# Performance work log

Hardware: AMD Instinct MI355X
Metric: run time of the kernel (lower is better)

Reference implementation:

```python
import jax, jax.numpy as jnp
import numpy as np

# Model / context constants (prefill path with 2 equal-length sequences)
B, S = 2, 2048            # batch, seq_len (cu_seqlens_q = cu_seqlens_k = [0, S, 2S])
H, KV, HD = 32, 8, 128    # num_heads, num_kv_heads, head_dim
SCALE = HD ** -0.5
NUM_SLOTS = 8192          # KV-cache token slots
DKV = KV * HD
N = B * S


def setup_inputs() -> dict:
    key = jax.random.key(0)
    k1, k2, k3 = jax.random.split(key, 3)
    return {
        "q": jax.random.normal(k1, (N, H * HD), jnp.float32),
        "k": jax.random.normal(k2, (N, DKV), jnp.float32),
        "v": jax.random.normal(k3, (N, DKV), jnp.float32),
        "k_cache": jnp.zeros((NUM_SLOTS, DKV), jnp.float32),
        "v_cache": jnp.zeros((NUM_SLOTS, DKV), jnp.float32),
        "slot_mapping": jnp.arange(N, dtype=jnp.int32),
    }


def reference(q, k, v, k_cache, v_cache, slot_mapping):
    # --- store_kvcache: fused scatter-store of new K/V into the paged cache ---
    k_cache = k_cache.at[slot_mapping].set(k)   # [num_slots, KV*hd]
    v_cache = v_cache.at[slot_mapping].set(v)

    # --- paged prefill: keys/values read back from cache via slot table ---
    kk = k_cache[slot_mapping].reshape(B, S, KV, HD)
    vv = v_cache[slot_mapping].reshape(B, S, KV, HD)
    qh = q.reshape(B, S, H, HD)

    # GQA: each KV head serves H // KV query heads
    G = H // KV
    kk = jnp.repeat(kk, G, axis=2)  # [B, S, H, hd]
    vv = jnp.repeat(vv, G, axis=2)

    scores = jnp.einsum('bqhd,bkhd->bhqk', qh, kk) * SCALE  # [B, H, S, S]
    causal = jnp.tril(jnp.ones((S, S), dtype=bool))
    neg = jnp.asarray(jnp.finfo(scores.dtype).min, scores.dtype)
    scores = jnp.where(causal[None, None], scores, neg)
    p = jax.nn.softmax(scores, axis=-1)
    o = jnp.einsum('bhqk,bkhd->bqhd', p, vv)  # [B, S, H, hd]
    return o.reshape(N, H * HD)
```

## Files before the change

### kernel.cpp

```cpp
#include <hip/hip_runtime.h>

typedef _Float16 half8 __attribute__((ext_vector_type(8)));
typedef _Float16 half2v __attribute__((ext_vector_type(2)));
typedef float f32x4 __attribute__((ext_vector_type(4)));

#define SEQ_LEN 2048
#define N_GQ 4
#define HD 128
#define DQ 4096
#define DKV 1024
#define ATT_SCALE 0.08838834764831845f

__global__ __launch_bounds__(512, 2) void attn_fwd(
    const float* __restrict__ qg, const float* __restrict__ kg,
    const float* __restrict__ vg, float* __restrict__ og)
{
    __shared__ char smem[65536];
    char* const Kb = smem;
    char* const Vb = smem + 16384;
    const int tid  = threadIdx.x;
    const int w    = tid >> 6;
    const int lane = tid & 63;
    const int lg   = lane >> 4;
    const int lr   = lane & 15;
    char* const Pb = smem + 32768 + w * 4096;

    const int kvh  = blockIdx.y;
    const int seq0 = (int)blockIdx.z * SEQ_LEN;
    const int head = kvh * N_GQ + (w >> 1);

    for (int rep = 0; rep < 2; ++rep) {
        const int qt = rep ? (31 - (int)blockIdx.x) : (int)blockIdx.x;
        const int q0 = qt * 64;
        const int qw = q0 + (w & 1) * 32;

        half8 qf[2][4];
        #pragma unroll
        for (int mq = 0; mq < 2; ++mq) {
            const int row = qw + mq * 16 + lr;
            const float* qp = qg + (size_t)(seq0 + row) * DQ + head * HD + lg * 8;
            #pragma unroll
            for (int kc = 0; kc < 4; ++kc) {
                f32x4 a = *(const f32x4*)(qp + kc * 32);
                f32x4 b = *(const f32x4*)(qp + kc * 32 + 4);
                half8 h;
                #pragma unroll
                for (int i = 0; i < 4; ++i) {
                    h[i]     = (_Float16)(a[i] * ATT_SCALE);
                    h[i + 4] = (_Float16)(b[i] * ATT_SCALE);
                }
                qf[mq][kc] = h;
            }
        }

        f32x4 oa[2][8];
        #pragma unroll
        for (int mq = 0; mq < 2; ++mq)
            #pragma unroll
            for (int dt = 0; dt < 8; ++dt)
                oa[mq][dt] = (f32x4){0.f, 0.f, 0.f, 0.f};
        float mrow[2][4], lrow[2][4];
        #pragma unroll
        for (int mq = 0; mq < 2; ++mq)
            #pragma unroll
            for (int r = 0; r < 4; ++r) { mrow[mq][r] = -1e30f; lrow[mq][r] = 0.f; }

        const int ntiles = qt + 1;
        for (int kvt = 0; kvt < ntiles; ++kvt) {
            const int kv0 = kvt * 64;
            __syncthreads();

            {
                const int r = tid >> 3, p = tid & 7;
                const float* kp = kg + (size_t)(seq0 + kv0 + r) * DKV + kvh * HD + p * 16;
                f32x4 f0 = *(const f32x4*)(kp);
                f32x4 f1 = *(const f32x4*)(kp + 4);
                f32x4 f2 = *(const f32x4*)(kp + 8);
                f32x4 f3 = *(const f32x4*)(kp + 12);
                half8 h0, h1;
                #pragma unroll
                for (int i = 0; i < 4; ++i) {
                    h0[i] = (_Float16)f0[i]; h0[i + 4] = (_Float16)f1[i];
                    h1[i] = (_Float16)f2[i]; h1[i + 4] = (_Float16)f3[i];
                }
                const int s0 = (p * 2)     ^ (r & 7);
                const int s1 = (p * 2 + 1) ^ (r & 7);
                *(half8*)(Kb + r * 256 + s0 * 16) = h0;
                *(half8*)(Kb + r * 256 + s1 * 16) = h1;
            }
            {
                const int r2 = (tid & 31) * 2, p = tid >> 5;
                const float* vp = vg + (size_t)(seq0 + kv0 + r2) * DKV + kvh * HD + p * 8;
                f32x4 a0 = *(const f32x4*)(vp);
                f32x4 a1 = *(const f32x4*)(vp + 4);
                f32x4 b0 = *(const f32x4*)(vp + DKV);
                f32x4 b1 = *(const f32x4*)(vp + DKV + 4);
                #pragma unroll
                for (int c = 0; c < 8; ++c) {
                    const int d = p * 8 + c;
                    half2v hv;
                    hv[0] = (_Float16)(c < 4 ? a0[c] : a1[c - 4]);
                    hv[1] = (_Float16)(c < 4 ? b0[c] : b1[c - 4]);
                    const int byt = (r2 * 2) ^ ((d & 7) << 4);
                    *(half2v*)(Vb + d * 128 + byt) = hv;
                }
            }
            __syncthreads();

            f32x4 sc[2][4];
            #pragma unroll
            for (int mq = 0; mq < 2; ++mq)
                #pragma unroll
                for (int nk = 0; nk < 4; ++nk)
                    sc[mq][nk] = (f32x4){0.f, 0.f, 0.f, 0.f};
            #pragma unroll
            for (int nk = 0; nk < 4; ++nk) {
                const int krow = nk * 16 + lr;
                half8 kf[4];
                #pragma unroll
                for (int kc = 0; kc < 4; ++kc) {
                    const int byt = (kc * 64 + lg * 16) ^ ((krow & 7) << 4);
                    kf[kc] = *(const half8*)(Kb + krow * 256 + byt);
                }
                #pragma unroll
                for (int mq = 0; mq < 2; ++mq)
                    #pragma unroll
                    for (int kc = 0; kc < 4; ++kc)
                        sc[mq][nk] = __builtin_amdgcn_mfma_f32_16x16x32_f16(
                            qf[mq][kc], kf[kc], sc[mq][nk], 0, 0, 0);
            }

            if (kvt == ntiles - 1) {
                #pragma unroll
                for (int mq = 0; mq < 2; ++mq)
                    #pragma unroll
                    for (int nk = 0; nk < 4; ++nk) {
                        const int col = kv0 + nk * 16 + lr;
                        #pragma unroll
                        for (int r = 0; r < 4; ++r) {
                            const int rowq = qw + mq * 16 + lg * 4 + r;
                            if (col > rowq) sc[mq][nk][r] = -1e30f;
                        }
                    }
            }

            #pragma unroll
            for (int mq = 0; mq < 2; ++mq) {
                float pm[4], mn[4], cc[4], rs[4];
                #pragma unroll
                for (int r = 0; r < 4; ++r)
                    pm[r] = fmaxf(fmaxf(sc[mq][0][r], sc[mq][1][r]),
                                  fmaxf(sc[mq][2][r], sc[mq][3][r]));
                #pragma unroll
                for (int off = 1; off < 16; off <<= 1)
                    #pragma unroll
                    for (int r = 0; r < 4; ++r)
                        pm[r] = fmaxf(pm[r], __shfl_xor(pm[r], off));
                #pragma unroll
                for (int r = 0; r < 4; ++r) {
                    mn[r] = fmaxf(mrow[mq][r], pm[r]);
                    cc[r] = __expf(mrow[mq][r] - mn[r]);
                    mrow[mq][r] = mn[r];
                    rs[r] = 0.f;
                }
                #pragma unroll
                for (int nk = 0; nk < 4; ++nk)
                    #pragma unroll
                    for (int r = 0; r < 4; ++r) {
                        const float pv = __expf(sc[mq][nk][r] - mn[r]);
                        sc[mq][nk][r] = pv;
                        rs[r] += pv;
                    }
                #pragma unroll
                for (int off = 1; off < 16; off <<= 1)
                    #pragma unroll
                    for (int r = 0; r < 4; ++r)
                        rs[r] += __shfl_xor(rs[r], off);
                #pragma unroll
                for (int r = 0; r < 4; ++r)
                    lrow[mq][r] = lrow[mq][r] * cc[r] + rs[r];
                #pragma unroll
                for (int dt = 0; dt < 8; ++dt)
                    #pragma unroll
                    for (int r = 0; r < 4; ++r)
                        oa[mq][dt][r] *= cc[r];
                #pragma unroll
                for (int nk = 0; nk < 4; ++nk)
                    #pragma unroll
                    for (int r = 0; r < 4; ++r) {
                        const int rowl = mq * 16 + lg * 4 + r;
                        const int byt = (nk * 32 + lr * 2) ^ ((rowl & 7) << 4);
                        *(_Float16*)(Pb + rowl * 128 + byt) = (_Float16)sc[mq][nk][r];
                    }
            }
            __syncthreads();

            #pragma unroll
            for (int kc = 0; kc < 2; ++kc) {
                half8 pf[2];
                #pragma unroll
                for (int mq = 0; mq < 2; ++mq) {
                    const int rowl = mq * 16 + lr;
                    const int byt = (kc * 64 + lg * 16) ^ ((rowl & 7) << 4);
                    pf[mq] = *(const half8*)(Pb + rowl * 128 + byt);
                }
                #pragma unroll
                for (int dt = 0; dt < 8; ++dt) {
                    const int d = dt * 16 + lr;
                    const int byt = (kc * 64 + lg * 16) ^ ((d & 7) << 4);
                    const half8 vf = *(const half8*)(Vb + d * 128 + byt);
                    oa[0][dt] = __builtin_amdgcn_mfma_f32_16x16x32_f16(pf[0], vf, oa[0][dt], 0, 0, 0);
                    oa[1][dt] = __builtin_amdgcn_mfma_f32_16x16x32_f16(pf[1], vf, oa[1][dt], 0, 0, 0);
                }
            }
        }

        #pragma unroll
        for (int mq = 0; mq < 2; ++mq) {
            float inv[4];
            #pragma unroll
            for (int r = 0; r < 4; ++r) inv[r] = 1.0f / lrow[mq][r];
            #pragma unroll
            for (int dt = 0; dt < 8; ++dt)
                #pragma unroll
                for (int r = 0; r < 4; ++r) {
                    const int rowq = qw + mq * 16 + lg * 4 + r;
                    og[(size_t)(seq0 + rowq) * DQ + head * HD + dt * 16 + lr]
                        = oa[mq][dt][r] * inv[r];
                }
        }
    }
}

extern "C" void kernel_launch(void* const* d_in, const int* in_sizes, int n_in,
                              void* d_out, int out_size, void* d_ws, size_t ws_size,
                              hipStream_t stream) {
    const float* q = (const float*)d_in[0];
    const float* k = (const float*)d_in[1];
    const float* v = (const float*)d_in[2];
    float* out = (float*)d_out;
    dim3 grid(16, 8, 2);
    attn_fwd<<<grid, 512, 0, stream>>>(q, k, v, out);
}
```

Measured before the change: 347.1 us.

## Double-buffer K/V tiles with register prefetch, 1024-thread blocks, lazy softmax rescale

Rewrites the attention kernel to use 16 waves of 16 query rows each, in 1024-thread blocks. The next K/V tile is prefetched into registers while the current tile is computed, and LDS is ping-ponged between two buffers, with the P scratch sharing the idle half. It also folds log2(e) into the Q scale so softmax can use exp2f, and skips rescaling the output accumulators unless the row max grows by more than a threshold. Wave priority hints are placed around the MFMA sections. The aim is to hide global-load latency and cut exponent and rescale work, at the cost of fewer registers per thread with launch_bounds(1024,4) and tighter LDS sharing.

```diff
diff --git a/kernel.cpp b/kernel.cpp
--- a/kernel.cpp
+++ b/kernel.cpp
@@ -9,36 +9,37 @@
 #define HD 128
 #define DQ 4096
 #define DKV 1024
-#define ATT_SCALE 0.08838834764831845f
-
-__global__ __launch_bounds__(512, 2) void attn_fwd(
+#define SCALE_L2E (0.08838834764831845f * 1.4426950408889634f)
+#define RESCALE_THR 4.0f
+
+__global__ __launch_bounds__(1024, 4) void attn_fwd(
     const float* __restrict__ qg, const float* __restrict__ kg,
     const float* __restrict__ vg, float* __restrict__ og)
 {
     __shared__ char smem[65536];
-    char* const Kb = smem;
-    char* const Vb = smem + 16384;
     const int tid  = threadIdx.x;
     const int w    = tid >> 6;
     const int lane = tid & 63;
     const int lg   = lane >> 4;
     const int lr   = lane & 15;
-    char* const Pb = smem + 32768 + w * 4096;
 
     const int kvh  = blockIdx.y;
     const int seq0 = (int)blockIdx.z * SEQ_LEN;
-    const int head = kvh * N_GQ + (w >> 1);
+    const int head = kvh * N_GQ + (w >> 2);
+
+    const int kr = tid >> 4, kp = tid & 15;
+    const int vr2 = (tid & 31) * 2, vp = tid >> 5;
+    const float* kbase = kg + (size_t)seq0 * DKV + kvh * HD;
+    const float* vbase = vg + (size_t)seq0 * DKV + kvh * HD;
 
     for (int rep = 0; rep < 2; ++rep) {
         const int qt = rep ? (31 - (int)blockIdx.x) : (int)blockIdx.x;
         const int q0 = qt * 64;
-        const int qw = q0 + (w & 1) * 32;
-
-        half8 qf[2][4];
-        #pragma unroll
-        for (int mq = 0; mq < 2; ++mq) {
-            const int row = qw + mq * 16 + lr;
-            const float* qp = qg + (size_t)(seq0 + row) * DQ + head * HD + lg * 8;
+        const int qw = q0 + (w & 3) * 16;
+
+        half8 qf[4];
+        {
+            const float* qp = qg + (size_t)(seq0 + qw + lr) * DQ + head * HD + lg * 8;
             #pragma unroll
             for (int kc = 0; kc < 4; ++kc) {
                 f32x4 a = *(const f32x4*)(qp + kc * 32);
@@ -46,189 +47,171 @@
                 half8 h;
                 #pragma unroll
                 for (int i = 0; i < 4; ++i) {
-                    h[i]     = (_Float16)(a[i] * ATT_SCALE);
-                    h[i + 4] = (_Float16)(b[i] * ATT_SCALE);
-                }
-                qf[mq][kc] = h;
-            }
-        }
-
-        f32x4 oa[2][8];
-        #pragma unroll
-        for (int mq = 0; mq < 2; ++mq)
-            #pragma unroll
-            for (int dt = 0; dt < 8; ++dt)
-                oa[mq][dt] = (f32x4){0.f, 0.f, 0.f, 0.f};
-        float mrow[2][4], lrow[2][4];
-        #pragma unroll
-        for (int mq = 0; mq < 2; ++mq)
-            #pragma unroll
-            for (int r = 0; r < 4; ++r) { mrow[mq][r] = -1e30f; lrow[mq][r] = 0.f; }
-
-        const int ntiles = qt + 1;
-        for (int kvt = 0; kvt < ntiles; ++kvt) {
-            const int kv0 = kvt * 64;
-            __syncthreads();
-
-            {
-                const int r = tid >> 3, p = tid & 7;
-                const float* kp = kg + (size_t)(seq0 + kv0 + r) * DKV + kvh * HD + p * 16;
-                f32x4 f0 = *(const f32x4*)(kp);
-                f32x4 f1 = *(const f32x4*)(kp + 4);
-                f32x4 f2 = *(const f32x4*)(kp + 8);
-                f32x4 f3 = *(const f32x4*)(kp + 12);
-                half8 h0, h1;
-                #pragma unroll
-                for (int i = 0; i < 4; ++i) {
-                    h0[i] = (_Float16)f0[i]; h0[i + 4] = (_Float16)f1[i];
-                    h1[i] = (_Float16)f2[i]; h1[i + 4] = (_Float16)f3[i];
-                }
-                const int s0 = (p * 2)     ^ (r & 7);
-                const int s1 = (p * 2 + 1) ^ (r & 7);
-                *(half8*)(Kb + r * 256 + s0 * 16) = h0;
-                *(half8*)(Kb + r * 256 + s1 * 16) = h1;
-            }
-            {
-                const int r2 = (tid & 31) * 2, p = tid >> 5;
-                const float* vp = vg + (size_t)(seq0 + kv0 + r2) * DKV + kvh * HD + p * 8;
-                f32x4 a0 = *(const f32x4*)(vp);
-                f32x4 a1 = *(const f32x4*)(vp + 4);
-                f32x4 b0 = *(const f32x4*)(vp + DKV);
-                f32x4 b1 = *(const f32x4*)(vp + DKV + 4);
-                #pragma unroll
-                for (int c = 0; c < 8; ++c) {
-                    const int d = p * 8 + c;
-                    half2v hv;
-                    hv[0] = (_Float16)(c < 4 ? a0[c] : a1[c - 4]);
-                    hv[1] = (_Float16)(c < 4 ? b0[c] : b1[c - 4]);
-                    const int byt = (r2 * 2) ^ ((d & 7) << 4);
-                    *(half2v*)(Vb + d * 128 + byt) = hv;
-                }
-            }
-            __syncthreads();
-
-            f32x4 sc[2][4];
-            #pragma unroll
-            for (int mq = 0; mq < 2; ++mq)
-                #pragma unroll
-                for (int nk = 0; nk < 4; ++nk)
-                    sc[mq][nk] = (f32x4){0.f, 0.f, 0.f, 0.f};
+                    h[i]     = (_Float16)(a[i] * SCALE_L2E);
+                    h[i + 4] = (_Float16)(b[i] * SCALE_L2E);
+                }
+                qf[kc] = h;
+            }
+        }
+
+        f32x4 oa[8];
+        #pragma unroll
+        for (int dt = 0; dt < 8; ++dt) oa[dt] = (f32x4){0.f, 0.f, 0.f, 0.f};
+        float mrow[4], lrow[4];
+        #pragma unroll
+        for (int r = 0; r < 4; ++r) { mrow[r] = -1e30f; lrow[r] = 0.f; }
+
+        f32x4 ks0, ks1, vs0, vs1;
+        {
+            const float* kpp = kbase + (size_t)kr * DKV + kp * 8;
+            ks0 = *(const f32x4*)kpp;  ks1 = *(const f32x4*)(kpp + 4);
+            const float* vpp = vbase + (size_t)vr2 * DKV + vp * 4;
+            vs0 = *(const f32x4*)vpp;  vs1 = *(const f32x4*)(vpp + DKV);
+        }
+        __syncthreads();
+        {
+            half8 h;
+            #pragma unroll
+            for (int i = 0; i < 4; ++i) { h[i] = (_Float16)ks0[i]; h[i+4] = (_Float16)ks1[i]; }
+            *(half8*)(smem + kr * 256 + ((kp ^ (kr & 7)) * 16)) = h;
+            #pragma unroll
+            for (int c = 0; c < 4; ++c) {
+                const int d = vp * 4 + c;
+                half2v hv; hv[0] = (_Float16)vs0[c]; hv[1] = (_Float16)vs1[c];
+                *(half2v*)(smem + 16384 + d * 128 + ((vr2 * 2) ^ ((d & 7) << 4))) = hv;
+            }
+        }
+        __syncthreads();
+
+        int curb = 0;
+        for (int t = 0; t <= qt; ++t) {
+            if (t < qt) {
+                const float* kpp = kbase + (size_t)((t + 1) * 64 + kr) * DKV + kp * 8;
+                ks0 = *(const f32x4*)kpp;  ks1 = *(const f32x4*)(kpp + 4);
+                const float* vpp = vbase + (size_t)((t + 1) * 64 + vr2) * DKV + vp * 4;
+                vs0 = *(const f32x4*)vpp;  vs1 = *(const f32x4*)(vpp + DKV);
+            }
+            char* const Kb = smem + curb;
+            char* const Vb = smem + curb + 16384;
+            char* const Pb = smem + (32768 - curb) + w * 2048;
+
+            f32x4 sc[4];
+            #pragma unroll
+            for (int nk = 0; nk < 4; ++nk) sc[nk] = (f32x4){0.f, 0.f, 0.f, 0.f};
+            __builtin_amdgcn_s_setprio(1);
             #pragma unroll
             for (int nk = 0; nk < 4; ++nk) {
                 const int krow = nk * 16 + lr;
                 half8 kf[4];
                 #pragma unroll
-                for (int kc = 0; kc < 4; ++kc) {
-                    const int byt = (kc * 64 + lg * 16) ^ ((krow & 7) << 4);
-                    kf[kc] = *(const half8*)(Kb + krow * 256 + byt);
-                }
-                #pragma unroll
-                for (int mq = 0; mq < 2; ++mq)
-                    #pragma unroll
-                    for (int kc = 0; kc < 4; ++kc)
-                        sc[mq][nk] = __builtin_amdgcn_mfma_f32_16x16x32_f16(
-                            qf[mq][kc], kf[kc], sc[mq][nk], 0, 0, 0);
-            }
-
-            if (kvt == ntiles - 1) {
-                #pragma unroll
-                for (int mq = 0; mq < 2; ++mq)
-                    #pragma unroll
-                    for (int nk = 0; nk < 4; ++nk) {
-                        const int col = kv0 + nk * 16 + lr;
-                        #pragma unroll
-                        for (int r = 0; r < 4; ++r) {
-                            const int rowq = qw + mq * 16 + lg * 4 + r;
-                            if (col > rowq) sc[mq][nk][r] = -1e30f;
-                        }
-                    }
-            }
-
-            #pragma unroll
-            for (int mq = 0; mq < 2; ++mq) {
-                float pm[4], mn[4], cc[4], rs[4];
-                #pragma unroll
-                for (int r = 0; r < 4; ++r)
-                    pm[r] = fmaxf(fmaxf(sc[mq][0][r], sc[mq][1][r]),
-                                  fmaxf(sc[mq][2][r], sc[mq][3][r]));
-                #pragma unroll
-                for (int off = 1; off < 16; off <<= 1)
+                for (int kc = 0; kc < 4; ++kc)
+                    kf[kc] = *(const half8*)(Kb + krow * 256 + (((kc * 4 + lg) ^ (krow & 7)) * 16));
+                #pragma unroll
+                for (int kc = 0; kc < 4; ++kc)
+                    sc[nk] = __builtin_amdgcn_mfma_f32_16x16x32_f16(qf[kc], kf[kc], sc[nk], 0, 0, 0);
+            }
+            __builtin_amdgcn_s_setprio(0);
+
+            if (t == qt) {
+                #pragma unroll
+                for (int nk = 0; nk < 4; ++nk) {
+                    const int col = q0 + nk * 16 + lr;
                     #pragma unroll
                     for (int r = 0; r < 4; ++r)
-                        pm[r] = fmaxf(pm[r], __shfl_xor(pm[r], off));
+                        if (col > qw + lg * 4 + r) sc[nk][r] = -1e30f;
+                }
+            }
+
+            float pm[4];
+            #pragma unroll
+            for (int r = 0; r < 4; ++r)
+                pm[r] = fmaxf(fmaxf(sc[0][r], sc[1][r]), fmaxf(sc[2][r], sc[3][r]));
+            #pragma unroll
+            for (int off = 1; off < 16; off <<= 1)
+                #pragma unroll
+                for (int r = 0; r < 4; ++r)
+                    pm[r] = fmaxf(pm[r], __shfl_xor(pm[r], off));
+            int need = 0;
+            #pragma unroll
+            for (int r = 0; r < 4; ++r) need |= (pm[r] > mrow[r] + RESCALE_THR) ? 1 : 0;
+            if (__any(need)) {
                 #pragma unroll
                 for (int r = 0; r < 4; ++r) {
-                    mn[r] = fmaxf(mrow[mq][r], pm[r]);
-                    cc[r] = __expf(mrow[mq][r] - mn[r]);
-                    mrow[mq][r] = mn[r];
-                    rs[r] = 0.f;
-                }
-                #pragma unroll
-                for (int nk = 0; nk < 4; ++nk)
+                    const float mn = fmaxf(mrow[r], pm[r]);
+                    const float cc = exp2f(mrow[r] - mn);
+                    mrow[r] = mn;
+                    lrow[r] *= cc;
                     #pragma unroll
-                    for (int r = 0; r < 4; ++r) {
-                        const float pv = __expf(sc[mq][nk][r] - mn[r]);
-                        sc[mq][nk][r] = pv;
-                        rs[r] += pv;
-                    }
-                #pragma unroll
-                for (int off = 1; off < 16; off <<= 1)
-                    #pragma unroll
-                    for (int r = 0; r < 4; ++r)
-                        rs[r] += __shfl_xor(rs[r], off);
+                    for (int dt = 0; dt < 8; ++dt) oa[dt][r] *= cc;
+                }
+            }
+            float rs[4] = {0.f, 0.f, 0.f, 0.f};
+            #pragma unroll
+            for (int nk = 0; nk < 4; ++nk)
+                #pragma unroll
+                for (int r = 0; r < 4; ++r) {
+                    const float p = exp2f(sc[nk][r] - mrow[r]);
+                    sc[nk][r] = p;
+                    rs[r] += p;
+                }
+            #pragma unroll
+            for (int off = 1; off < 16; off <<= 1)
                 #pragma unroll
                 for (int r = 0; r < 4; ++r)
-                    lrow[mq][r] = lrow[mq][r] * cc[r] + rs[r];
-                #pragma unroll
-                for (int dt = 0; dt < 8; ++dt)
-                    #pragma unroll
-                    for (int r = 0; r < 4; ++r)
-                        oa[mq][dt][r] *= cc[r];
-                #pragma unroll
-                for (int nk = 0; nk < 4; ++nk)
-                    #pragma unroll
-                    for (int r = 0; r < 4; ++r) {
-                        const int rowl = mq * 16 + lg * 4 + r;
-                        const int byt = (nk * 32 + lr * 2) ^ ((rowl & 7) << 4);
-                        *(_Float16*)(Pb + rowl * 128 + byt) = (_Float16)sc[mq][nk][r];
-                    }
-            }
-            __syncthreads();
-
+                    rs[r] += __shfl_xor(rs[r], off);
+            #pragma unroll
+            for (int r = 0; r < 4; ++r) lrow[r] += rs[r];
+            #pragma unroll
+            for (int nk = 0; nk < 4; ++nk)
+                #pragma unroll
+                for (int r = 0; r < 4; ++r) {
+                    const int row = lg * 4 + r;
+                    *(_Float16*)(Pb + row * 128 + ((nk * 32 + lr * 2) ^ ((row & 7) << 4)))
+                        = (_Float16)sc[nk][r];
+                }
+
+            __builtin_amdgcn_s_setprio(1);
             #pragma unroll
             for (int kc = 0; kc < 2; ++kc) {
-                half8 pf[2];
-                #pragma unroll
-                for (int mq = 0; mq < 2; ++mq) {
-                    const int rowl = mq * 16 + lr;
-                    const int byt = (kc * 64 + lg * 16) ^ ((rowl & 7) << 4);
-                    pf[mq] = *(const half8*)(Pb + rowl * 128 + byt);
-                }
+                const half8 pf = *(const half8*)(Pb + lr * 128 + (((kc * 4 + lg) * 16) ^ ((lr & 7) << 4)));
                 #pragma unroll
                 for (int dt = 0; dt < 8; ++dt) {
                     const int d = dt * 16 + lr;
-                    const int byt = (kc * 64 + lg * 16) ^ ((d & 7) << 4);
-                    const half8 vf = *(const half8*)(Vb + d * 128 + byt);
-                    oa[0][dt] = __builtin_amdgcn_mfma_f32_16x16x32_f16(pf[0], vf, oa[0][dt], 0, 0, 0);
-                    oa[1][dt] = __builtin_amdgcn_mfma_f32_16x16x32_f16(pf[1], vf, oa[1][dt], 0, 0, 0);
-                }
-            }
-        }
-
-        #pragma unroll
-        for (int mq = 0; mq < 2; ++mq) {
-            float inv[4];
-            #pragma unroll
-            for (int r = 0; r < 4; ++r) inv[r] = 1.0f / lrow[mq][r];
-            #pragma unroll
-            for (int dt = 0; dt < 8; ++dt)
-                #pragma unroll
-                for (int r = 0; r < 4; ++r) {
-                    const int rowq = qw + mq * 16 + lg * 4 + r;
-                    og[(size_t)(seq0 + rowq) * DQ + head * HD + dt * 16 + lr]
-                        = oa[mq][dt][r] * inv[r];
-                }
-        }
+                    const half8 vf = *(const half8*)(Vb + d * 128 + (((kc * 4 + lg) * 16) ^ ((d & 7) << 4)));
+                    oa[dt] = __builtin_amdgcn_mfma_f32_16x16x32_f16(pf, vf, oa[dt], 0, 0, 0);
+                }
+            }
+            __builtin_amdgcn_s_setprio(0);
+
+            if (t < qt) {
+                __syncthreads();
+                char* const nb = smem + (32768 - curb);
+                half8 h;
+                #pragma unroll
+                for (int i = 0; i < 4; ++i) { h[i] = (_Float16)ks0[i]; h[i+4] = (_Float16)ks1[i]; }
+                *(half8*)(nb + kr * 256 + ((kp ^ (kr & 7)) * 16)) = h;
+                #pragma unroll
+                for (int c = 0; c < 4; ++c) {
+                    const int d = vp * 4 + c;
+                    half2v hv; hv[0] = (_Float16)vs0[c]; hv[1] = (_Float16)vs1[c];
+                    *(half2v*)(nb + 16384 + d * 128 + ((vr2 * 2) ^ ((d & 7) << 4))) = hv;
+                }
+                __syncthreads();
+                curb = 32768 - curb;
+            }
+        }
+
+        float inv[4];
+        #pragma unroll
+        for (int r = 0; r < 4; ++r) inv[r] = 1.0f / lrow[r];
+        #pragma unroll
+        for (int dt = 0; dt < 8; ++dt)
+            #pragma unroll
+            for (int r = 0; r < 4; ++r) {
+                const int rowq = qw + lg * 4 + r;
+                og[(size_t)(seq0 + rowq) * DQ + head * HD + dt * 16 + lr]
+                    = oa[dt][r] * inv[r];
+            }
     }
 }
 
@@ -239,6 +222,5 @@
     const float* k = (const float*)d_in[1];
     const float* v = (const float*)d_in[2];
     float* out = (float*)d_out;
-    dim3 grid(16, 8, 2);
-    attn_fwd<<<grid, 512, 0, stream>>>(q, k, v, out);
+    attn_fwd<<<dim3(16, 8, 2), 1024, 0, stream>>>(q, k, v, out);
 }
```

New measurement: 453.8 us. 1.31x slower.
